# Kernel optimization log

Hardware: AMD Instinct MI355X
Metric: run time of the kernel (lower is better)

Reference implementation:

```python
import jax, jax.numpy as jnp
import numpy as np

LATENT = 64
HEADS = 4
N_A, N_B = 1024, 1024


def setup_inputs() -> dict:
    key = jax.random.key(0)
    ks = jax.random.split(key, 10)
    L = LATENT
    return {
        "rho_real": jax.random.normal(ks[0], (N_A, N_B), dtype=jnp.float32),
        "rho_imag": jax.random.normal(ks[1], (N_A, N_B), dtype=jnp.float32),
        "l_A": jax.random.randint(ks[2], (N_A,), 0, 3),
        "l_B": jax.random.randint(ks[3], (N_B,), 0, 3),
        "Z_A": 6,
        "Z_B": 8,
        # block_encoder: Linear(2, 64) -> SiLU -> Linear(64, latent_dim)
        "W1": jax.random.normal(ks[4], (64, 2), dtype=jnp.float32) * 0.5,
        "b1": jnp.zeros((64,), dtype=jnp.float32),
        "W2": jax.random.normal(ks[5], (L, 64), dtype=jnp.float32) * 0.1,
        "b2": jnp.zeros((L,), dtype=jnp.float32),
        # learned pooling query (1, latent_dim)
        "query": jax.random.normal(ks[6], (1, L), dtype=jnp.float32),
        # nn.MultiheadAttention packed in-projection and out-projection
        "in_proj_w": jax.random.normal(ks[7], (3 * L, L), dtype=jnp.float32) * 0.1,
        "in_proj_b": jnp.zeros((3 * L,), dtype=jnp.float32),
        "out_proj_w": jax.random.normal(ks[8], (L, L), dtype=jnp.float32) * 0.1,
        "out_proj_b": jnp.zeros((L,), dtype=jnp.float32),
    }


def reference(rho_real, rho_imag, l_A, l_B, Z_A, Z_B,
              W1, b1, W2, b2, query, in_proj_w, in_proj_b,
              out_proj_w, out_proj_b):
    L = query.shape[-1]
    H = HEADS
    hd = L // H
    # Batched equivalent of the per-(i,j) loop: all n_A*n_B elements at once.
    x = jnp.stack([rho_real.reshape(-1), rho_imag.reshape(-1)], axis=-1)  # [N, 2]
    h = jax.nn.silu(x @ W1.T + b1) @ W2.T + b2                            # [N, L]
    # MultiheadAttention with single query (batch=1, tgt_len=1, src_len=N)
    Wq, Wk, Wv = in_proj_w[:L], in_proj_w[L:2 * L], in_proj_w[2 * L:]
    bq, bk, bv = in_proj_b[:L], in_proj_b[L:2 * L], in_proj_b[2 * L:]
    q = (query @ Wq.T + bq).reshape(H, hd)        # [H, hd]
    k = (h @ Wk.T + bk).reshape(-1, H, hd)        # [N, H, hd]
    v = (h @ Wv.T + bv).reshape(-1, H, hd)        # [N, H, hd]
    scale = 1.0 / jnp.sqrt(jnp.asarray(hd, dtype=x.dtype))
    scores = jnp.einsum('hd,nhd->hn', q, k) * scale   # [H, N]
    attn = jax.nn.softmax(scores, axis=-1)
    pooled = jnp.einsum('hn,nhd->hd', attn, v).reshape(L)  # [L]
    return pooled @ out_proj_w.T + out_proj_b             # [latent_dim]
```

## Files before the change

### kernel.cpp

```cpp
#include <hip/hip_runtime.h>


#define LOG2E 1.44269504088896340736f
#define NLN2  (-0.69314718055994530942f)

#if __has_builtin(__builtin_amdgcn_exp2f)
#define EXP2(x) __builtin_amdgcn_exp2f(x)
#else
#define EXP2(x) exp2f(x)
#endif
#if __has_builtin(__builtin_amdgcn_rcpf)
#define RCP(x) __builtin_amdgcn_rcpf(x)
#else
#define RCP(x) (1.0f / (x))
#endif

#define WS_C4   0
#define WS_G4   256
#define WS_D    512
#define WS_ACC  768
#define NSLOT      32
#define SLOTSTRIDE 272

#define NPTS       (1024 * 1024)
#define NGROUPS    (NPTS / 64)
#define K1_BLOCKS  2048
#define K1_THREADS 128
#define WAVES_TOTAL (K1_BLOCKS * (K1_THREADS / 64))
#define GROUPS_PER_WAVE (NGROUPS / WAVES_TOTAL)

#define WG_FENCE() __builtin_amdgcn_fence(__ATOMIC_ACQ_REL, "workgroup")

__global__ void setup_kernel(const float* __restrict__ W1, const float* __restrict__ b1,
                             const float* __restrict__ W2, const float* __restrict__ b2,
                             const float* __restrict__ query,
                             const float* __restrict__ ipw, const float* __restrict__ ipb,
                             float* __restrict__ ws)
{
    __shared__ float qs[64];
    __shared__ float as[4 * 64];
    const int t = threadIdx.x;

    if (t < 64) {
        float acc = ipb[t];
        for (int k = 0; k < 64; ++k) acc += ipw[t * 64 + k] * query[k];
        qs[t] = acc;
    }
    __syncthreads();

    {
        const int h = t >> 6, k = t & 63;
        float acc = 0.0f;
        for (int m = 0; m < 16; ++m)
            acc += ipw[(64 + h * 16 + m) * 64 + k] * qs[h * 16 + m];
        as[h * 64 + k] = 0.25f * acc;
    }
    __syncthreads();

    if (t < 64) {
        const int j = t;
        for (int h = 0; h < 4; ++h) {
            float g = 0.0f;
            for (int d = 0; d < 64; ++d) g += as[h * 64 + d] * W2[d * 64 + j];
            ws[WS_G4 + j * 4 + h] = LOG2E * g;
        }
        ws[WS_C4 + j * 4 + 0] = -LOG2E * W1[2 * j];
        ws[WS_C4 + j * 4 + 1] = -LOG2E * W1[2 * j + 1];
        ws[WS_C4 + j * 4 + 2] = -LOG2E * b1[j];
        ws[WS_C4 + j * 4 + 3] = 0.0f;
    }
    if (t < 4) {
        float d = 0.0f;
        for (int c = 0; c < 64; ++c) d += as[t * 64 + c] * b2[c];
        float qb = 0.0f;
        for (int m = 0; m < 16; ++m) qb += qs[t * 16 + m] * ipb[64 + t * 16 + m];
        ws[WS_D + t] = LOG2E * (d + 0.25f * qb);
    }
}

__global__ __launch_bounds__(K1_THREADS) void main_kernel(
        const float* __restrict__ rr, const float* __restrict__ ri,
        const float4* __restrict__ c4g, const float4* __restrict__ g4g,
        const float* __restrict__ dvec, float* __restrict__ accb)
{
    __shared__ unsigned short us[2][64 * 66];
    __shared__ float4 p4s[2][64];

    const int t    = threadIdx.x;
    const int lane = t & 63;
    const int w    = t >> 6;

    const float d0 = dvec[0], d1 = dvec[1], d2 = dvec[2], d3 = dvec[3];

    const int gwave = blockIdx.x * 2 + w;
    float l0 = 0, l1 = 0, l2 = 0, l3 = 0;
    float t0 = 0, t1 = 0, t2 = 0, t3 = 0;
    unsigned short* uw = us[w];

    for (int it = 0; it < GROUPS_PER_WAVE; ++it) {
        const int g   = gwave + it * WAVES_TOTAL;
        const int idx = g * 64 + lane;
        const float r  = rr[idx];
        const float im = ri[idx];

        float s0 = d0, s1 = d1, s2 = d2, s3 = d3;
        #pragma unroll 16
        for (int j = 0; j < 64; ++j) {
            const float4 c  = c4g[j];
            const float4 gg = g4g[j];
            const float zn = fmaf(c.x, r, fmaf(c.y, im, c.z));
            const float e  = EXP2(zn);
            const float rc = RCP(1.0f + e);
            const float u  = zn * NLN2 * rc;
            s0 = fmaf(gg.x, u, s0);
            s1 = fmaf(gg.y, u, s1);
            s2 = fmaf(gg.z, u, s2);
            s3 = fmaf(gg.w, u, s3);
            uw[j * 66 + lane] =
                (unsigned short)((__float_as_uint(u) + 0x8000u) >> 16);
        }
        const float p0 = EXP2(s0), p1 = EXP2(s1), p2 = EXP2(s2), p3 = EXP2(s3);
        l0 += p0; l1 += p1; l2 += p2; l3 += p3;
        p4s[w][lane] = make_float4(p0, p1, p2, p3);
        WG_FENCE();

        const unsigned int* urow = (const unsigned int*)(uw + lane * 66);
        #pragma unroll 16
        for (int p2 = 0; p2 < 32; ++p2) {
            const unsigned int bits = urow[p2];
            const float ulo = __uint_as_float(bits << 16);
            const float uhi = __uint_as_float(bits & 0xFFFF0000u);
            const float4 pa = p4s[w][2 * p2];
            const float4 pb = p4s[w][2 * p2 + 1];
            t0 = fmaf(pa.x, ulo, t0); t0 = fmaf(pb.x, uhi, t0);
            t1 = fmaf(pa.y, ulo, t1); t1 = fmaf(pb.y, uhi, t1);
            t2 = fmaf(pa.z, ulo, t2); t2 = fmaf(pb.z, uhi, t2);
            t3 = fmaf(pa.w, ulo, t3); t3 = fmaf(pb.w, uhi, t3);
        }
        WG_FENCE();
    }

    for (int m = 1; m < 64; m <<= 1) {
        l0 += __shfl_xor(l0, m);
        l1 += __shfl_xor(l1, m);
        l2 += __shfl_xor(l2, m);
        l3 += __shfl_xor(l3, m);
    }

    float* acc = accb + (blockIdx.x & (NSLOT - 1)) * SLOTSTRIDE;
    if (lane == 0) {
        atomicAdd(acc + 0, l0);
        atomicAdd(acc + 1, l1);
        atomicAdd(acc + 2, l2);
        atomicAdd(acc + 3, l3);
    }
    atomicAdd(acc + 4 + 0 * 64 + lane, t0);
    atomicAdd(acc + 4 + 1 * 64 + lane, t1);
    atomicAdd(acc + 4 + 2 * 64 + lane, t2);
    atomicAdd(acc + 4 + 3 * 64 + lane, t3);
}

__global__ void finish_kernel(const float* __restrict__ W2, const float* __restrict__ b2,
                              const float* __restrict__ ipw, const float* __restrict__ ipb,
                              const float* __restrict__ opw, const float* __restrict__ opb,
                              const float* __restrict__ ws, float* __restrict__ out)
{
    __shared__ float red[260];
    __shared__ float sb[256];
    __shared__ float pl[64];
    const int t = threadIdx.x;

    {
        float a = 0.0f;
        for (int s = 0; s < NSLOT; ++s) a += ws[WS_ACC + s * SLOTSTRIDE + t];
        red[t] = a;
        if (t < 4) {
            float a2 = 0.0f;
            for (int s = 0; s < NSLOT; ++s) a2 += ws[WS_ACC + s * SLOTSTRIDE + 256 + t];
            red[256 + t] = a2;
        }
    }
    __syncthreads();

    {
        const int h = t >> 6, j = t & 63;
        const float inv = 1.0f / red[h];
        float a = 0.0f;
        for (int k = 0; k < 64; ++k) a += W2[j * 64 + k] * red[4 + h * 64 + k];
        sb[t] = fmaf(inv, a, b2[j]);
    }
    __syncthreads();

    if (t < 64) {
        const int h = t >> 4;
        float a = ipb[128 + t];
        for (int d = 0; d < 64; ++d) a += ipw[(128 + t) * 64 + d] * sb[h * 64 + d];
        pl[t] = a;
    }
    __syncthreads();

    if (t < 64) {
        float a = opb[t];
        for (int p = 0; p < 64; ++p) a += opw[t * 64 + p] * pl[p];
        out[t] = a;
    }
}

extern "C" void kernel_launch(void* const* d_in, const int* in_sizes, int n_in,
                              void* d_out, int out_size, void* d_ws, size_t ws_size,
                              hipStream_t stream)
{
    const float* rr  = (const float*)d_in[0];
    const float* ri  = (const float*)d_in[1];
    const float* W1  = (const float*)d_in[6];
    const float* b1  = (const float*)d_in[7];
    const float* W2  = (const float*)d_in[8];
    const float* b2  = (const float*)d_in[9];
    const float* qy  = (const float*)d_in[10];
    const float* ipw = (const float*)d_in[11];
    const float* ipb = (const float*)d_in[12];
    const float* opw = (const float*)d_in[13];
    const float* opb = (const float*)d_in[14];
    float* ws  = (float*)d_ws;
    float* out = (float*)d_out;

    hipMemsetAsync(ws + WS_ACC, 0, (size_t)NSLOT * SLOTSTRIDE * sizeof(float), stream);
    setup_kernel<<<1, 256, 0, stream>>>(W1, b1, W2, b2, qy, ipw, ipb, ws);
    main_kernel<<<K1_BLOCKS, K1_THREADS, 0, stream>>>(
        rr, ri,
        (const float4*)(ws + WS_C4), (const float4*)(ws + WS_G4),
        ws + WS_D, ws + WS_ACC);
    finish_kernel<<<1, 256, 0, stream>>>(W2, b2, ipw, ipb, opw, opb, ws, out);
}
```

Measured before the change: 139.2 us.

## Use bf16 MFMA for weighted-sum accumulation and fuse finish into main kernel

The per-lane scalar FMA loop that accumulates attention-weighted hidden activations is replaced by bf16 MFMA 16x16x32 instructions. The probabilities are now also stored as bf16 in LDS. The finish kernel is folded into the main kernel through a last-block atomic counter, and setup is spread across 64 blocks using shuffle reductions. This targets the VALU-heavy accumulation and the extra kernel launches, at the cost of lower precision for p and a serialized tail in the last block.

```diff
diff --git a/kernel.cpp b/kernel.cpp
--- a/kernel.cpp
+++ b/kernel.cpp
@@ -15,21 +15,29 @@
 #define RCP(x) (1.0f / (x))
 #endif
 
+typedef __attribute__((ext_vector_type(8))) __bf16 bf16x8;
+typedef __attribute__((ext_vector_type(4))) float  f32x4;
+
 #define WS_C4   0
 #define WS_G4   256
 #define WS_D    512
 #define WS_ACC  768
 #define NSLOT      32
 #define SLOTSTRIDE 272
+#define WS_CNT  (WS_ACC + NSLOT * SLOTSTRIDE)
 
 #define NPTS       (1024 * 1024)
 #define NGROUPS    (NPTS / 64)
 #define K1_BLOCKS  2048
 #define K1_THREADS 128
-#define WAVES_TOTAL (K1_BLOCKS * (K1_THREADS / 64))
+#define WAVES_TOTAL (K1_BLOCKS * 2)
 #define GROUPS_PER_WAVE (NGROUPS / WAVES_TOTAL)
 
 #define WG_FENCE() __builtin_amdgcn_fence(__ATOMIC_ACQ_REL, "workgroup")
+
+__device__ __forceinline__ unsigned short to_bf16(float x) {
+    return (unsigned short)((__float_as_uint(x) + 0x8000u) >> 16);
+}
 
 __global__ void setup_kernel(const float* __restrict__ W1, const float* __restrict__ b1,
                              const float* __restrict__ W2, const float* __restrict__ b2,
@@ -37,65 +45,89 @@
                              const float* __restrict__ ipw, const float* __restrict__ ipb,
                              float* __restrict__ ws)
 {
-    __shared__ float qs[64];
-    __shared__ float as[4 * 64];
+    __shared__ float qv[64], qs[64], as4[4][64];
     const int t = threadIdx.x;
-
-    if (t < 64) {
-        float acc = ipb[t];
-        for (int k = 0; k < 64; ++k) acc += ipw[t * 64 + k] * query[k];
-        qs[t] = acc;
-    }
+    const int b = blockIdx.x;
+
+    qv[t] = query[t];
     __syncthreads();
 
     {
-        const int h = t >> 6, k = t & 63;
-        float acc = 0.0f;
+        float a = ipb[t];
+        #pragma unroll
+        for (int k = 0; k < 64; ++k) a = fmaf(ipw[t * 64 + k], qv[k], a);
+        qs[t] = a;
+    }
+    __syncthreads();
+
+    #pragma unroll
+    for (int h = 0; h < 4; ++h) {
+        float a = 0.0f;
+        #pragma unroll
         for (int m = 0; m < 16; ++m)
-            acc += ipw[(64 + h * 16 + m) * 64 + k] * qs[h * 16 + m];
-        as[h * 64 + k] = 0.25f * acc;
-    }
-    __syncthreads();
-
-    if (t < 64) {
-        const int j = t;
-        for (int h = 0; h < 4; ++h) {
-            float g = 0.0f;
-            for (int d = 0; d < 64; ++d) g += as[h * 64 + d] * W2[d * 64 + j];
-            ws[WS_G4 + j * 4 + h] = LOG2E * g;
-        }
-        ws[WS_C4 + j * 4 + 0] = -LOG2E * W1[2 * j];
-        ws[WS_C4 + j * 4 + 1] = -LOG2E * W1[2 * j + 1];
-        ws[WS_C4 + j * 4 + 2] = -LOG2E * b1[j];
-        ws[WS_C4 + j * 4 + 3] = 0.0f;
-    }
-    if (t < 4) {
+            a = fmaf(ipw[(64 + h * 16 + m) * 64 + t], qs[h * 16 + m], a);
+        as4[h][t] = 0.25f * a;
+    }
+    __syncthreads();
+
+    const float w2 = W2[t * 64 + b];
+    float g[4];
+    #pragma unroll
+    for (int h = 0; h < 4; ++h) {
+        float v = as4[h][t] * w2;
+        for (int m = 1; m < 64; m <<= 1) v += __shfl_xor(v, m);
+        g[h] = v;
+    }
+    if (t == 0) {
+        ws[WS_G4 + b * 4 + 0] = LOG2E * g[0];
+        ws[WS_G4 + b * 4 + 1] = LOG2E * g[1];
+        ws[WS_G4 + b * 4 + 2] = LOG2E * g[2];
+        ws[WS_G4 + b * 4 + 3] = LOG2E * g[3];
+        ws[WS_C4 + b * 4 + 0] = -LOG2E * W1[2 * b];
+        ws[WS_C4 + b * 4 + 1] = -LOG2E * W1[2 * b + 1];
+        ws[WS_C4 + b * 4 + 2] = -LOG2E * b1[b];
+        ws[WS_C4 + b * 4 + 3] = 0.0f;
+    }
+    if (b == 0 && t < 4) {
         float d = 0.0f;
-        for (int c = 0; c < 64; ++c) d += as[t * 64 + c] * b2[c];
+        #pragma unroll
+        for (int c = 0; c < 64; ++c) d += as4[t][c] * b2[c];
         float qb = 0.0f;
+        #pragma unroll
         for (int m = 0; m < 16; ++m) qb += qs[t * 16 + m] * ipb[64 + t * 16 + m];
         ws[WS_D + t] = LOG2E * (d + 0.25f * qb);
     }
 }
 
-__global__ __launch_bounds__(K1_THREADS) void main_kernel(
+__global__ __launch_bounds__(K1_THREADS, 4) void main_kernel(
         const float* __restrict__ rr, const float* __restrict__ ri,
         const float4* __restrict__ c4g, const float4* __restrict__ g4g,
-        const float* __restrict__ dvec, float* __restrict__ accb)
+        const float* __restrict__ dvec, float* __restrict__ accb, int* __restrict__ cnt,
+        const float* __restrict__ W2, const float* __restrict__ b2,
+        const float* __restrict__ ipw, const float* __restrict__ ipb,
+        const float* __restrict__ opw, const float* __restrict__ opb,
+        float* __restrict__ out)
 {
-    __shared__ unsigned short us[2][64 * 66];
-    __shared__ float4 p4s[2][64];
+    __shared__ __align__(16) unsigned short us[2][64 * 72];
+    __shared__ __align__(16) unsigned short ps[2][4 * 72];
 
     const int t    = threadIdx.x;
     const int lane = t & 63;
     const int w    = t >> 6;
+    const int quad = lane >> 4;
+
+    unsigned short* uw = us[w];
+    unsigned short* pw = ps[w];
 
     const float d0 = dvec[0], d1 = dvec[1], d2 = dvec[2], d3 = dvec[3];
 
     const int gwave = blockIdx.x * 2 + w;
     float l0 = 0, l1 = 0, l2 = 0, l3 = 0;
-    float t0 = 0, t1 = 0, t2 = 0, t3 = 0;
-    unsigned short* uw = us[w];
+    f32x4 acc[4];
+    #pragma unroll
+    for (int i = 0; i < 4; ++i) acc[i] = (f32x4){0.f, 0.f, 0.f, 0.f};
+
+    const unsigned short* pa = pw + (lane & 3) * 72 + quad * 8;
 
     for (int it = 0; it < GROUPS_PER_WAVE; ++it) {
         const int g   = gwave + it * WAVES_TOTAL;
@@ -116,26 +148,25 @@
             s1 = fmaf(gg.y, u, s1);
             s2 = fmaf(gg.z, u, s2);
             s3 = fmaf(gg.w, u, s3);
-            uw[j * 66 + lane] =
-                (unsigned short)((__float_as_uint(u) + 0x8000u) >> 16);
+            uw[j * 72 + lane] = to_bf16(u);
         }
         const float p0 = EXP2(s0), p1 = EXP2(s1), p2 = EXP2(s2), p3 = EXP2(s3);
         l0 += p0; l1 += p1; l2 += p2; l3 += p3;
-        p4s[w][lane] = make_float4(p0, p1, p2, p3);
+        pw[0 * 72 + lane] = to_bf16(p0);
+        pw[1 * 72 + lane] = to_bf16(p1);
+        pw[2 * 72 + lane] = to_bf16(p2);
+        pw[3 * 72 + lane] = to_bf16(p3);
         WG_FENCE();
 
-        const unsigned int* urow = (const unsigned int*)(uw + lane * 66);
-        #pragma unroll 16
-        for (int p2 = 0; p2 < 32; ++p2) {
-            const unsigned int bits = urow[p2];
-            const float ulo = __uint_as_float(bits << 16);
-            const float uhi = __uint_as_float(bits & 0xFFFF0000u);
-            const float4 pa = p4s[w][2 * p2];
-            const float4 pb = p4s[w][2 * p2 + 1];
-            t0 = fmaf(pa.x, ulo, t0); t0 = fmaf(pb.x, uhi, t0);
-            t1 = fmaf(pa.y, ulo, t1); t1 = fmaf(pb.y, uhi, t1);
-            t2 = fmaf(pa.z, ulo, t2); t2 = fmaf(pb.z, uhi, t2);
-            t3 = fmaf(pa.w, ulo, t3); t3 = fmaf(pb.w, uhi, t3);
+        const bf16x8 a0 = *(const bf16x8*)(pa);
+        const bf16x8 a1 = *(const bf16x8*)(pa + 32);
+        #pragma unroll
+        for (int tt = 0; tt < 4; ++tt) {
+            const unsigned short* bb = uw + (tt * 16 + (lane & 15)) * 72 + quad * 8;
+            acc[tt] = __builtin_amdgcn_mfma_f32_16x16x32_bf16(
+                          a0, *(const bf16x8*)(bb), acc[tt], 0, 0, 0);
+            acc[tt] = __builtin_amdgcn_mfma_f32_16x16x32_bf16(
+                          a1, *(const bf16x8*)(bb + 32), acc[tt], 0, 0, 0);
         }
         WG_FENCE();
     }
@@ -147,53 +178,59 @@
         l3 += __shfl_xor(l3, m);
     }
 
-    float* acc = accb + (blockIdx.x & (NSLOT - 1)) * SLOTSTRIDE;
+    float* accS = accb + (blockIdx.x & (NSLOT - 1)) * SLOTSTRIDE;
     if (lane == 0) {
-        atomicAdd(acc + 0, l0);
-        atomicAdd(acc + 1, l1);
-        atomicAdd(acc + 2, l2);
-        atomicAdd(acc + 3, l3);
-    }
-    atomicAdd(acc + 4 + 0 * 64 + lane, t0);
-    atomicAdd(acc + 4 + 1 * 64 + lane, t1);
-    atomicAdd(acc + 4 + 2 * 64 + lane, t2);
-    atomicAdd(acc + 4 + 3 * 64 + lane, t3);
-}
-
-__global__ void finish_kernel(const float* __restrict__ W2, const float* __restrict__ b2,
-                              const float* __restrict__ ipw, const float* __restrict__ ipb,
-                              const float* __restrict__ opw, const float* __restrict__ opb,
-                              const float* __restrict__ ws, float* __restrict__ out)
-{
-    __shared__ float red[260];
-    __shared__ float sb[256];
-    __shared__ float pl[64];
-    const int t = threadIdx.x;
-
-    {
+        atomicAdd(accS + 0, l0);
+        atomicAdd(accS + 1, l1);
+        atomicAdd(accS + 2, l2);
+        atomicAdd(accS + 3, l3);
+    }
+    if (lane < 16) {
+        #pragma unroll
+        for (int tt = 0; tt < 4; ++tt)
+            #pragma unroll
+            for (int r2 = 0; r2 < 4; ++r2)
+                atomicAdd(accS + 4 + r2 * 64 + tt * 16 + lane, acc[tt][r2]);
+    }
+
+    __threadfence();
+    __syncthreads();
+    __shared__ int isLast;
+    if (t == 0) {
+        const int old = atomicAdd(cnt, 1);
+        isLast = (old == K1_BLOCKS - 1);
+    }
+    __syncthreads();
+    if (!isLast) return;
+    __threadfence();
+
+    float* red = (float*)&us[0][0];
+    float* sb  = red + 260;
+    float* pl  = sb + 256;
+
+    for (int idx = t; idx < 260; idx += K1_THREADS) {
         float a = 0.0f;
-        for (int s = 0; s < NSLOT; ++s) a += ws[WS_ACC + s * SLOTSTRIDE + t];
-        red[t] = a;
-        if (t < 4) {
-            float a2 = 0.0f;
-            for (int s = 0; s < NSLOT; ++s) a2 += ws[WS_ACC + s * SLOTSTRIDE + 256 + t];
-            red[256 + t] = a2;
-        }
-    }
-    __syncthreads();
-
-    {
-        const int h = t >> 6, j = t & 63;
+        for (int s = 0; s < NSLOT; ++s)
+            a += __hip_atomic_load(accb + s * SLOTSTRIDE + idx,
+                                   __ATOMIC_RELAXED, __HIP_MEMORY_SCOPE_AGENT);
+        red[idx] = a;
+    }
+    __syncthreads();
+
+    for (int idx = t; idx < 256; idx += K1_THREADS) {
+        const int h = idx >> 6, j = idx & 63;
         const float inv = 1.0f / red[h];
         float a = 0.0f;
+        #pragma unroll
         for (int k = 0; k < 64; ++k) a += W2[j * 64 + k] * red[4 + h * 64 + k];
-        sb[t] = fmaf(inv, a, b2[j]);
+        sb[idx] = fmaf(inv, a, b2[j]);
     }
     __syncthreads();
 
     if (t < 64) {
         const int h = t >> 4;
         float a = ipb[128 + t];
+        #pragma unroll
         for (int d = 0; d < 64; ++d) a += ipw[(128 + t) * 64 + d] * sb[h * 64 + d];
         pl[t] = a;
     }
@@ -201,6 +238,7 @@
 
     if (t < 64) {
         float a = opb[t];
+        #pragma unroll
         for (int p = 0; p < 64; ++p) a += opw[t * 64 + p] * pl[p];
         out[t] = a;
     }
@@ -224,11 +262,11 @@
     float* ws  = (float*)d_ws;
     float* out = (float*)d_out;
 
-    hipMemsetAsync(ws + WS_ACC, 0, (size_t)NSLOT * SLOTSTRIDE * sizeof(float), stream);
-    setup_kernel<<<1, 256, 0, stream>>>(W1, b1, W2, b2, qy, ipw, ipb, ws);
+    hipMemsetAsync(ws + WS_ACC, 0, (size_t)(NSLOT * SLOTSTRIDE + 1) * sizeof(float), stream);
+    setup_kernel<<<64, 64, 0, stream>>>(W1, b1, W2, b2, qy, ipw, ipb, ws);
     main_kernel<<<K1_BLOCKS, K1_THREADS, 0, stream>>>(
         rr, ri,
-        (const float4*)(ws + WS_C4), (const float4*)(ws + WS_G4),
-        ws + WS_D, ws + WS_ACC);
-    finish_kernel<<<1, 256, 0, stream>>>(W2, b2, ipw, ipb, opw, opb, ws, out);
-}
+        (const float4*)(ws + WS_C4), (const float4*)(ws + WS_G4), ws + WS_D,
+        ws + WS_ACC, (int*)(ws + WS_CNT),
+        W2, b2, ipw, ipb, opw, opb, out);
+}
```

Result: slower. 178.1 us (+28.0%).
